# Performance work log

Measured on AMD Instinct MI355X. Metric: run time of the kernel, lower is better.

Reference implementation:

```python
import jax, jax.numpy as jnp
import numpy as np

PS = 8        # window/patch size (win_size)
STRIDE = 4    # overlapping-window stride
HEADS = 2


def _rel_pos_index(ps):
    ch = np.arange(ps)
    coords = np.stack(np.meshgrid(ch, ch, indexing='ij'))  # (2, ps, ps)
    cf = coords.reshape(2, -1)
    rel = cf[:, :, None] - cf[:, None, :]                   # (2, L, L)
    rel = rel.transpose(1, 2, 0).copy()
    rel[:, :, 0] += ps - 1
    rel[:, :, 1] += ps - 1
    rel[:, :, 0] *= 2 * ps - 1
    return rel.sum(-1).astype(np.int32)                     # (L, L)


def setup_inputs() -> dict:
    key = jax.random.key(0)
    ks = jax.random.split(key, 6)
    t, h, w, c = 8, 128, 128, 32
    inp = {
        'x': jax.random.normal(ks[0], (t, h, w, c), jnp.float32),
        'qkv_w': jax.random.normal(ks[1], (3 * c, c), jnp.float32) * (c ** -0.5),
        'qkv_b': jnp.zeros((3 * c,), jnp.float32),
        'rel_pos_table': jax.random.normal(ks[2], ((2 * PS - 1) ** 2, HEADS), jnp.float32) * 0.02,
        'proj_w': jax.random.normal(ks[3], (c, c), jnp.float32) * (c ** -0.5),
        'proj_b': jnp.zeros((c,), jnp.float32),
        'rel_pos_index': jnp.asarray(_rel_pos_index(PS)),
    }
    return inp


def reference(x, qkv_w, qkv_b, rel_pos_table, proj_w, proj_b, rel_pos_index):
    t, h, w, c = x.shape
    hd = c // HEADS
    scale = hd ** -0.5
    L = PS * PS
    nh = (h - 1) // STRIDE + 1
    nw = (w - 1) // STRIDE + 1

    # --- iUnfold: gather overlapping ps x ps patches with reflected borders ---
    r0 = jnp.arange(nh) * STRIDE
    c0 = jnp.arange(nw) * STRIDE
    ridx = r0[:, None] + jnp.arange(PS)[None, :]            # (nh, ps)
    cidx = c0[:, None] + jnp.arange(PS)[None, :]            # (nw, ps)
    ridx = jnp.where(ridx >= h, 2 * (h - 1) - ridx, ridx)
    cidx = jnp.where(cidx >= w, 2 * (w - 1) - cidx, cidx)
    # advanced indexing -> (t, nh, nw, ps, ps, c)
    patches = x[:, ridx[:, None, :, None], cidx[None, :, None, :], :]
    n = t * nh * nw
    patches = patches.reshape(n, L, c)

    # --- LinearProjection qkv ---
    qkv = patches @ qkv_w.T + qkv_b                          # (n, L, 3c)
    q, k, v = jnp.split(qkv, 3, axis=-1)
    def heads(a):
        return a.reshape(n, L, HEADS, hd).transpose(0, 2, 1, 3)  # (n, H, L, hd)
    q, k, v = heads(q), heads(k), heads(v)

    # --- scaled attention + indexed relative position bias ---
    attn = jnp.einsum('nhld,nhmd->nhlm', q * scale, k)       # (n, H, L, L)
    bias = rel_pos_table[rel_pos_index]                      # (L, L, H)
    attn = jax.nn.softmax(attn + bias.transpose(2, 0, 1)[None], axis=-1)
    out = jnp.einsum('nhlm,nhmd->nhld', attn, v)             # (n, H, L, hd)
    out = out.transpose(0, 2, 1, 3).reshape(n, L, c)
    out = out @ proj_w.T + proj_b

    # --- iFold: scatter-add with overlap-count (wfold) normalization ---
    lin = (ridx[:, None, :, None] * w + cidx[None, :, None, :]).reshape(-1)  # (nh*nw*L,)
    vals = out.reshape(t, nh * nw * L, c)
    vid = jnp.zeros((t, h * w, c), x.dtype).at[:, lin, :].add(vals)
    cnt = jnp.zeros((h * w,), x.dtype).at[lin].add(1.0)
    vid = vid / (cnt[None, :, None] + 1e-10)
    return vid.reshape(t, h, w, c)
```

## Files before the change

### kernel.cpp

```cpp
#include <hip/hip_runtime.h>
#include <hip/hip_bf16.h>
#include <stdint.h>

typedef __attribute__((ext_vector_type(8))) short bf16x8;
typedef __attribute__((ext_vector_type(4))) float f32x4;

#define LOG2E 1.44269504088896340736f
#define QSCALE (0.25f * LOG2E)

#define WS_BIASF 0u
#define WS_QKVW  32768u
#define WS_PROJW 38912u
#define WS_QKVB  40960u
#define WS_OUT   41472u
#define NEED_FULL (41472ull + 8192ull*64*32*2)

#define PWAVE 4096

__device__ __forceinline__ uint32_t pk2(float a, float b){
    union{__hip_bfloat162 h;uint32_t u;}c;
    c.h=__float22bfloat162_rn(make_float2(a,b)); return c.u;
}
template<int OFF>
__device__ __forceinline__ uint2 tr16(uint32_t a){
    uint2 d;
    asm volatile("ds_read_b64_tr_b16 %0, %1 offset:%2" : "=v"(d) : "v"(a), "i"(OFF) : "memory");
    return d;
}
__device__ __forceinline__ void lgkm0(){
    asm volatile("s_waitcnt lgkmcnt(0)" ::: "memory");
    __builtin_amdgcn_sched_barrier(0);
}
__device__ __forceinline__ bf16x8 mk8u(uint2 a, uint2 b){
    union{bf16x8 v;uint32_t u[4];}z; z.u[0]=a.x; z.u[1]=a.y; z.u[2]=b.x; z.u[3]=b.y; return z.v;
}
__device__ __forceinline__ bf16x8 mk8q(uint32_t q0, uint32_t q1, uint32_t q2, uint32_t q3){
    union{bf16x8 v;uint32_t u[4];}z; z.u[0]=q0; z.u[1]=q1; z.u[2]=q2; z.u[3]=q3; return z.v;
}
__device__ __forceinline__ void pl32(uint32_t &a, uint32_t &b){
    asm volatile("v_permlane32_swap_b32 %0, %1" : "+v"(a), "+v"(b));
}
__device__ __forceinline__ void pl16(uint32_t &a, uint32_t &b){
    asm volatile("v_permlane16_swap_b32 %0, %1" : "+v"(a), "+v"(b));
}
__device__ __forceinline__ f32x4 mfma16(uint2 a, uint2 b, f32x4 c){
    asm("v_mfma_f32_16x16x16_bf16 %0, %1, %2, %0" : "+v"(c) : "v"(a), "v"(b));
    return c;
}

__global__ __launch_bounds__(256) void prep(const float* __restrict__ qkv_w,
                                            const float* __restrict__ qkv_b,
                                            const float* __restrict__ rel_tab,
                                            const float* __restrict__ proj_w,
                                            char* __restrict__ ws)
{
    int t = blockIdx.x*256 + threadIdx.x;
    if (t < 2048) {
        int lanei = t & 63, tile = t >> 6;
        int h = tile >> 4, nt = (tile >> 2) & 3, mt = tile & 3;
        int gg = lanei >> 4, lnn = lanei & 15;
        int l = 16*nt + lnn;
        f32x4 v;
        #pragma unroll
        for (int r = 0; r < 4; ++r) {
            int m = 16*mt + 4*gg + r;
            int dr = (l >> 3) - (m >> 3) + 7;
            int dc = (l & 7) - (m & 7) + 7;
            v[r] = rel_tab[(dr*15 + dc)*2 + h] * LOG2E;
        }
        *(f32x4*)(ws + WS_BIASF + (size_t)t*16) = v;
    } else if (t < 3584) {
        int e = (t - 2048) * 2;
        int row = e >> 5;
        float s = (row < 32) ? QSCALE : 1.0f;
        *(uint32_t*)(ws + WS_QKVW + e*2) = pk2(qkv_w[e]*s, qkv_w[e+1]*s);
    } else {
        int e = (t - 3584) * 2;
        *(uint32_t*)(ws + WS_PROJW + e*2) = pk2(proj_w[e], proj_w[e+1]);
    }
    if (t < 96) {
        float s = (t < 32) ? QSCALE : 1.0f;
        ((float*)(ws + WS_QKVB))[t] = qkv_b[t] * s;
    }
}

template<int WSPATH>
__global__ __launch_bounds__(128, 3) void win_attn(
    const float* __restrict__ x, const float* __restrict__ proj_b,
    const char* __restrict__ wsc, uint16_t* __restrict__ wout,
    float* __restrict__ out)
{
    __shared__ __align__(16) char smem_all[2*PWAVE];
    const int tid = threadIdx.x;
    const int wv = tid >> 6, lane = tid & 63;
    const int g = lane >> 4, ln = lane & 15;
    const int bid = blockIdx.x;
    const int sb = (bid & 7) * 512 + (bid >> 3);
    const int wid = sb * 2 + wv;
    const int t_i = wid >> 10, wi = (wid >> 5) & 31, wj = wid & 31;
    char* smem = smem_all + wv * PWAVE;
    const uint32_t Lb = (uint32_t)(uintptr_t)(&smem[0]);

    const f32x4* biasF = (const f32x4*)(wsc + WS_BIASF);
    const uint16_t* wbf = (const uint16_t*)(wsc + WS_QKVW);
    const float* qbs = (const float*)(wsc + WS_QKVB);

    int pixb[4];
    #pragma unroll
    for (int i = 0; i < 4; ++i) {
        int tok = 16*i + ln, pr = tok >> 3, pc = tok & 7;
        int ar = wi*4 + pr; if (ar >= 128) ar = 254 - ar;
        int ac = wj*4 + pc; if (ac >= 128) ac = 254 - ac;
        pixb[i] = (t_i*128 + ar)*128 + ac;
    }

    bf16x8 xf[4];
    #pragma unroll
    for (int nt = 0; nt < 4; ++nt) {
        const float4* p = (const float4*)(x + (size_t)pixb[nt]*32 + 8*g);
        float4 a = p[0], b = p[1];
        union{bf16x8 v; uint32_t u[4];} z;
        z.u[0]=pk2(a.x,a.y); z.u[1]=pk2(a.z,a.w);
        z.u[2]=pk2(b.x,b.y); z.u[3]=pk2(b.z,b.w);
        xf[nt] = z.v;
    }

    uint2 qk[4][4];
    #pragma unroll
    for (int mt = 0; mt < 6; ++mt) {
        bf16x8 wf = *(const bf16x8*)(wbf + (ln + 16*mt)*32 + 8*g);
        float4 qb = *(const float4*)(qbs + 16*mt + 4*g);
        #pragma unroll
        for (int nt = 0; nt < 4; ++nt) {
            f32x4 acc = {qb.x, qb.y, qb.z, qb.w};
            acc = __builtin_amdgcn_mfma_f32_16x16x32_bf16(wf, xf[nt], acc, 0, 0, 0);
            if (mt < 4) {
                qk[mt][nt].x = pk2(acc[0], acc[1]);
                qk[mt][nt].y = pk2(acc[2], acc[3]);
            } else {
                int tok = 16*nt + ln;
                uint2 u; u.x = pk2(acc[0], acc[1]); u.y = pk2(acc[2], acc[3]);
                *(uint2*)(smem + (mt-4)*2048 + tok*32 + 8*g) = u;
            }
        }
    }

    const uint32_t one2 = 0x3f803f80u;
    const bf16x8 ones = mk8q(one2, one2, one2, one2);

    #pragma unroll
    for (int h = 0; h < 2; ++h) {
        f32x4 bp[16];
        #pragma unroll
        for (int t2 = 0; t2 < 16; ++t2)
            bp[t2] = biasF[(h*16 + t2)*64 + lane];

        uint32_t va = Lb + h*2048 + 256*g + 8*ln;
        uint2 v00 = tr16<0>(va),    v01 = tr16<128>(va);
        uint2 v10 = tr16<1024>(va), v11 = tr16<1152>(va);
        lgkm0();
        bf16x8 vb0 = mk8u(v00, v01), vb1 = mk8u(v10, v11);

        #pragma unroll
        for (int nt = 0; nt < 4; ++nt) {
            __builtin_amdgcn_s_setprio(1);
            f32x4 sc[4];
            #pragma unroll
            for (int mt = 0; mt < 4; ++mt)
                sc[mt] = mfma16(qk[2+h][mt], qk[h][nt], bp[nt*4 + mt]);
            __builtin_amdgcn_s_setprio(0);

            #pragma unroll
            for (int mt = 0; mt < 4; ++mt) {
                sc[mt][0]=__builtin_amdgcn_exp2f(sc[mt][0]);
                sc[mt][1]=__builtin_amdgcn_exp2f(sc[mt][1]);
                sc[mt][2]=__builtin_amdgcn_exp2f(sc[mt][2]);
                sc[mt][3]=__builtin_amdgcn_exp2f(sc[mt][3]);
            }

            uint32_t pkA[4], pkB[4];
            #pragma unroll
            for (int mt = 0; mt < 4; ++mt) {
                pkA[mt] = pk2(sc[mt][0], sc[mt][1]);
                pkB[mt] = pk2(sc[mt][2], sc[mt][3]);
            }
            uint32_t a0 = pkA[0], a1 = pkA[1]; pl32(a0, a1); pl16(a0, a1);
            uint32_t b0 = pkB[0], b1 = pkB[1]; pl32(b0, b1); pl16(b0, b1);
            bf16x8 pa0 = mk8q(a0, b0, a1, b1);
            uint32_t a2 = pkA[2], a3 = pkA[3]; pl32(a2, a3); pl16(a2, a3);
            uint32_t b2 = pkB[2], b3 = pkB[3]; pl32(b2, b3); pl16(b2, b3);
            bf16x8 pa1 = mk8q(a2, b2, a3, b3);

            __builtin_amdgcn_s_setprio(1);
            f32x4 z = {0.f,0.f,0.f,0.f};
            z = __builtin_amdgcn_mfma_f32_16x16x32_bf16(pa0, vb0, z, 0, 0, 0);
            f32x4 oc = __builtin_amdgcn_mfma_f32_16x16x32_bf16(pa1, vb1, z, 0, 0, 0);
            f32x4 sm = {0.f,0.f,0.f,0.f};
            sm = __builtin_amdgcn_mfma_f32_16x16x32_bf16(pa0, ones, sm, 0, 0, 0);
            sm = __builtin_amdgcn_mfma_f32_16x16x32_bf16(pa1, ones, sm, 0, 0, 0);
            __builtin_amdgcn_s_setprio(0);

            oc[0] *= __builtin_amdgcn_rcpf(sm[0]);
            oc[1] *= __builtin_amdgcn_rcpf(sm[1]);
            oc[2] *= __builtin_amdgcn_rcpf(sm[2]);
            oc[3] *= __builtin_amdgcn_rcpf(sm[3]);

            uint2 u; u.x = pk2(oc[0], oc[1]); u.y = pk2(oc[2], oc[3]);
            *(uint2*)(smem + h*2048 + (nt*4 + (ln>>2))*128 + (ln&3)*32 + 8*g) = u;
        }
    }

    uint32_t ob = Lb + ((uint32_t)(g >> 1) << 11) + ((uint32_t)(g & 1) << 8) + 8*ln;
    uint2 a0=tr16<0>(ob),    a1=tr16<128>(ob);
    uint2 b0=tr16<512>(ob),  b1=tr16<640>(ob);
    uint2 c0=tr16<1024>(ob), c1=tr16<1152>(ob);
    uint2 d0=tr16<1536>(ob), d1=tr16<1664>(ob);
    lgkm0();
    bf16x8 oa[4];
    oa[0]=mk8u(a0,a1); oa[1]=mk8u(b0,b1); oa[2]=mk8u(c0,c1); oa[3]=mk8u(d0,d1);

    if (WSPATH) {
        #pragma unroll
        for (int nt = 0; nt < 4; ++nt)
            *(bf16x8*)(wout + ((size_t)wid*64 + 16*nt + ln)*32 + 8*g) = oa[nt];
    } else {
        const uint16_t* pwbf = (const uint16_t*)(wsc + WS_PROJW);
        bf16x8 w2f[2];
        w2f[0] = *(const bf16x8*)(pwbf + ln*32 + 8*g);
        w2f[1] = *(const bf16x8*)(pwbf + (16 + ln)*32 + 8*g);
        float4 pbv[2];
        pbv[0] = *(const float4*)(proj_b + 4*g);
        pbv[1] = *(const float4*)(proj_b + 16 + 4*g);
        #pragma unroll
        for (int mt2 = 0; mt2 < 2; ++mt2) {
            #pragma unroll
            for (int nt = 0; nt < 4; ++nt) {
                f32x4 acc = {pbv[mt2].x, pbv[mt2].y, pbv[mt2].z, pbv[mt2].w};
                acc = __builtin_amdgcn_mfma_f32_16x16x32_bf16(w2f[mt2], oa[nt], acc, 0, 0, 0);
                #pragma unroll
                for (int r = 0; r < 4; ++r)
                    atomicAdd(out + (size_t)pixb[nt]*32 + 16*mt2 + 4*g + r, acc[r]);
            }
        }
    }
}

__global__ __launch_bounds__(256) void finish_kernel(const uint16_t* __restrict__ ws,
                                                     const char* __restrict__ wsc,
                                                     const float* __restrict__ proj_b,
                                                     float* __restrict__ out)
{
    __shared__ __align__(16) char smem[20480];
    const int tid = threadIdx.x;
    const int wv = tid >> 6, lane = tid & 63;
    const int g = lane >> 4, ln = lane & 15;
    const int pix0 = (blockIdx.x * 4 + wv) * 64;
    const int p = pix0 + lane;
    const int c = p & 127, r = (p >> 7) & 127, t_i = p >> 14;
    char* Ls = smem + wv * 5120;

    float s[32];
    #pragma unroll
    for (int q = 0; q < 32; ++q) s[q] = 0.f;

    int wr[3], pr[3], nr = 0;
    { int w0 = r >> 2;
      wr[0]=w0; pr[0]=r&3; nr=1;
      if (w0 >= 1) { wr[nr]=w0-1; pr[nr]=(r&3)+4; nr++; }
      if (r >= 123 && r <= 126) { wr[nr]=31; pr[nr]=130-r; nr++; } }
    int wc[3], pc[3], nc = 0;
    { int w0 = c >> 2;
      wc[0]=w0; pc[0]=c&3; nc=1;
      if (w0 >= 1) { wc[nc]=w0-1; pc[nc]=(c&3)+4; nc++; }
      if (c >= 123 && c <= 126) { wc[nc]=31; pc[nc]=130-c; nc++; } }

    #pragma unroll
    for (int i = 0; i < 3; ++i) {
        #pragma unroll
        for (int j = 0; j < 3; ++j) {
            if (i < nr && j < nc) {
                int win = t_i*1024 + wr[i]*32 + wc[j];
                int tok = pr[i]*8 + pc[j];
                const uint32_t* ab = (const uint32_t*)(ws + ((size_t)win*64 + tok)*32);
                #pragma unroll
                for (int q = 0; q < 16; ++q) {
                    uint32_t u = ab[q];
                    union{uint32_t uu; float f;} lo, hi;
                    lo.uu = u << 16; hi.uu = u & 0xffff0000u;
                    s[2*q]   += lo.f;
                    s[2*q+1] += hi.f;
                }
            }
        }
    }
    float inv = __builtin_amdgcn_rcpf((float)(nr*nc));
    #pragma unroll
    for (int q = 0; q < 4; ++q) {
        uint4 u;
        u.x = pk2(s[8*q+0]*inv, s[8*q+1]*inv);
        u.y = pk2(s[8*q+2]*inv, s[8*q+3]*inv);
        u.z = pk2(s[8*q+4]*inv, s[8*q+5]*inv);
        u.w = pk2(s[8*q+6]*inv, s[8*q+7]*inv);
        *(uint4*)(Ls + lane*80 + 16*q) = u;
    }
    __syncthreads();
    const uint16_t* pwbf = (const uint16_t*)(wsc + WS_PROJW);
    bf16x8 w2f[2];
    w2f[0] = *(const bf16x8*)(pwbf + ln*32 + 8*g);
    w2f[1] = *(const bf16x8*)(pwbf + (16 + ln)*32 + 8*g);
    float4 pbv[2];
    pbv[0] = *(const float4*)(proj_b + 4*g);
    pbv[1] = *(const float4*)(proj_b + 16 + 4*g);
    bf16x8 oa[4];
    #pragma unroll
    for (int nt = 0; nt < 4; ++nt)
        oa[nt] = *(const bf16x8*)(Ls + (ln + 16*nt)*80 + 16*g);
    #pragma unroll
    for (int mt2 = 0; mt2 < 2; ++mt2) {
        #pragma unroll
        for (int nt = 0; nt < 4; ++nt) {
            f32x4 acc = {pbv[mt2].x, pbv[mt2].y, pbv[mt2].z, pbv[mt2].w};
            acc = __builtin_amdgcn_mfma_f32_16x16x32_bf16(w2f[mt2], oa[nt], acc, 0, 0, 0);
            *(f32x4*)(out + (size_t)(pix0 + 16*nt + ln)*32 + 16*mt2 + 4*g) = acc;
        }
    }
}

__global__ __launch_bounds__(256) void div_kernel(float* __restrict__ out)
{
    int gid = blockIdx.x*blockDim.x + threadIdx.x;
    const int total4 = 8*128*128*32/4;
    if (gid >= total4) return;
    int pix = gid >> 3;
    int c_ = pix % 128;
    int r_ = (pix / 128) % 128;
    int cr = 0, cc = 0;
    for (int i = 0; i < 32; ++i) {
        #pragma unroll
        for (int p = 0; p < 8; ++p) {
            int rr = i*4 + p; if (rr >= 128) rr = 254 - rr;
            cr += (rr == r_);
            int aa = i*4 + p; if (aa >= 128) aa = 254 - aa;
            cc += (aa == c_);
        }
    }
    float inv = 1.f / ((float)cr*(float)cc + 1e-10f);
    float4* p4 = reinterpret_cast<float4*>(out) + gid;
    float4 v = *p4;
    v.x *= inv; v.y *= inv; v.z *= inv; v.w *= inv;
    *p4 = v;
}

extern "C" void kernel_launch(void* const* d_in, const int* in_sizes, int n_in,
                              void* d_out, int out_size, void* d_ws, size_t ws_size,
                              hipStream_t stream) {
    const float* x       = (const float*)d_in[0];
    const float* qkv_w   = (const float*)d_in[1];
    const float* qkv_b   = (const float*)d_in[2];
    const float* rel_tab = (const float*)d_in[3];
    const float* proj_w  = (const float*)d_in[4];
    const float* proj_b  = (const float*)d_in[5];
    float* out = (float*)d_out;
    char* ws = (char*)d_ws;

    prep<<<16, 256, 0, stream>>>(qkv_w, qkv_b, rel_tab, proj_w, ws);

    if (ws_size >= NEED_FULL) {
        win_attn<1><<<4096, 128, 0, stream>>>(x, proj_b, (const char*)ws,
                                              (uint16_t*)(ws + WS_OUT), out);
        finish_kernel<<<512, 256, 0, stream>>>((const uint16_t*)(ws + WS_OUT),
                                               (const char*)ws, proj_b, out);
    } else {
        hipMemsetAsync(out, 0, (size_t)out_size*sizeof(float), stream);
        win_attn<0><<<4096, 128, 0, stream>>>(x, proj_b, (const char*)ws, nullptr, out);
        const int tot4 = 8*128*128*32/4;
        div_kernel<<<(tot4 + 255)/256, 256, 0, stream>>>(out);
    }
}
```

Baseline: 51.20 us.

## Process two windows per wave and fold V bias after softmax normalization

Each wave now handles two attention windows instead of one. Weight fragments and relative-position bias loads are shared across both windows, and bias loads are software-prefetched one tile ahead instead of all 16 being held in registers. The V bias is dropped from the V projection and added after normalization, which is exact because softmax rows sum to one. Registers per wave roughly double, so launch bounds drop to 2 blocks per SIMD and the grid is halved, trading occupancy for more independent MFMA work per wave.

```diff
diff --git a/kernel.cpp b/kernel.cpp
--- a/kernel.cpp
+++ b/kernel.cpp
@@ -15,7 +15,7 @@
 #define WS_OUT   41472u
 #define NEED_FULL (41472ull + 8192ull*64*32*2)
 
-#define PWAVE 4096
+#define PWIN 4096
 
 __device__ __forceinline__ uint32_t pk2(float a, float b){
     union{__hip_bfloat162 h;uint32_t u;}c;
@@ -85,62 +85,76 @@
 }
 
 template<int WSPATH>
-__global__ __launch_bounds__(128, 3) void win_attn(
+__global__ __launch_bounds__(128, 2) void win_attn(
     const float* __restrict__ x, const float* __restrict__ proj_b,
     const char* __restrict__ wsc, uint16_t* __restrict__ wout,
     float* __restrict__ out)
 {
-    __shared__ __align__(16) char smem_all[2*PWAVE];
+    __shared__ __align__(16) char smem_all[4*PWIN];
     const int tid = threadIdx.x;
     const int wv = tid >> 6, lane = tid & 63;
     const int g = lane >> 4, ln = lane & 15;
     const int bid = blockIdx.x;
-    const int sb = (bid & 7) * 512 + (bid >> 3);
-    const int wid = sb * 2 + wv;
-    const int t_i = wid >> 10, wi = (wid >> 5) & 31, wj = wid & 31;
-    char* smem = smem_all + wv * PWAVE;
-    const uint32_t Lb = (uint32_t)(uintptr_t)(&smem[0]);
+    const int sb = (bid & 7) * 256 + (bid >> 3);
+    const int wid0 = sb*4 + wv*2;
+    char* wbase = smem_all + wv * 2 * PWIN;
+    const uint32_t Lb = (uint32_t)(uintptr_t)(&wbase[0]);
 
     const f32x4* biasF = (const f32x4*)(wsc + WS_BIASF);
     const uint16_t* wbf = (const uint16_t*)(wsc + WS_QKVW);
     const float* qbs = (const float*)(wsc + WS_QKVB);
 
-    int pixb[4];
-    #pragma unroll
-    for (int i = 0; i < 4; ++i) {
-        int tok = 16*i + ln, pr = tok >> 3, pc = tok & 7;
-        int ar = wi*4 + pr; if (ar >= 128) ar = 254 - ar;
-        int ac = wj*4 + pc; if (ac >= 128) ac = 254 - ac;
-        pixb[i] = (t_i*128 + ar)*128 + ac;
-    }
-
-    bf16x8 xf[4];
-    #pragma unroll
-    for (int nt = 0; nt < 4; ++nt) {
-        const float4* p = (const float4*)(x + (size_t)pixb[nt]*32 + 8*g);
-        float4 a = p[0], b = p[1];
-        union{bf16x8 v; uint32_t u[4];} z;
-        z.u[0]=pk2(a.x,a.y); z.u[1]=pk2(a.z,a.w);
-        z.u[2]=pk2(b.x,b.y); z.u[3]=pk2(b.z,b.w);
-        xf[nt] = z.v;
-    }
-
-    uint2 qk[4][4];
+    int pixb[2][4];
+    #pragma unroll
+    for (int w = 0; w < 2; ++w) {
+        const int wid = wid0 + w;
+        const int t_i = wid >> 10, wi = (wid >> 5) & 31, wj = wid & 31;
+        #pragma unroll
+        for (int i = 0; i < 4; ++i) {
+            int tok = 16*i + ln, pr = tok >> 3, pc = tok & 7;
+            int ar = wi*4 + pr; if (ar >= 128) ar = 254 - ar;
+            int ac = wj*4 + pc; if (ac >= 128) ac = 254 - ac;
+            pixb[w][i] = (t_i*128 + ar)*128 + ac;
+        }
+    }
+
+    bf16x8 xf[2][4];
+    #pragma unroll
+    for (int w = 0; w < 2; ++w) {
+        #pragma unroll
+        for (int nt = 0; nt < 4; ++nt) {
+            const float4* p = (const float4*)(x + (size_t)pixb[w][nt]*32 + 8*g);
+            float4 a = p[0], b = p[1];
+            union{bf16x8 v; uint32_t u[4];} z;
+            z.u[0]=pk2(a.x,a.y); z.u[1]=pk2(a.z,a.w);
+            z.u[2]=pk2(b.x,b.y); z.u[3]=pk2(b.z,b.w);
+            xf[w][nt] = z.v;
+        }
+    }
+
+    const f32x4 zero4 = {0.f, 0.f, 0.f, 0.f};
+
+    uint2 qk[2][4][4];
     #pragma unroll
     for (int mt = 0; mt < 6; ++mt) {
         bf16x8 wf = *(const bf16x8*)(wbf + (ln + 16*mt)*32 + 8*g);
         float4 qb = *(const float4*)(qbs + 16*mt + 4*g);
         #pragma unroll
-        for (int nt = 0; nt < 4; ++nt) {
-            f32x4 acc = {qb.x, qb.y, qb.z, qb.w};
-            acc = __builtin_amdgcn_mfma_f32_16x16x32_bf16(wf, xf[nt], acc, 0, 0, 0);
-            if (mt < 4) {
-                qk[mt][nt].x = pk2(acc[0], acc[1]);
-                qk[mt][nt].y = pk2(acc[2], acc[3]);
-            } else {
-                int tok = 16*nt + ln;
-                uint2 u; u.x = pk2(acc[0], acc[1]); u.y = pk2(acc[2], acc[3]);
-                *(uint2*)(smem + (mt-4)*2048 + tok*32 + 8*g) = u;
+        for (int w = 0; w < 2; ++w) {
+            #pragma unroll
+            for (int nt = 0; nt < 4; ++nt) {
+                f32x4 acc;
+                if (mt < 4) { acc[0]=qb.x; acc[1]=qb.y; acc[2]=qb.z; acc[3]=qb.w; }
+                else        { acc = zero4; }
+                acc = __builtin_amdgcn_mfma_f32_16x16x32_bf16(wf, xf[w][nt], acc, 0, 0, 0);
+                if (mt < 4) {
+                    qk[w][mt][nt].x = pk2(acc[0], acc[1]);
+                    qk[w][mt][nt].y = pk2(acc[2], acc[3]);
+                } else {
+                    int tok = 16*nt + ln;
+                    uint2 u; u.x = pk2(acc[0], acc[1]); u.y = pk2(acc[2], acc[3]);
+                    *(uint2*)(wbase + w*PWIN + (mt-4)*2048 + tok*32 + 8*g) = u;
+                }
             }
         }
     }
@@ -150,96 +164,130 @@
 
     #pragma unroll
     for (int h = 0; h < 2; ++h) {
-        f32x4 bp[16];
-        #pragma unroll
-        for (int t2 = 0; t2 < 16; ++t2)
-            bp[t2] = biasF[(h*16 + t2)*64 + lane];
-
-        uint32_t va = Lb + h*2048 + 256*g + 8*ln;
-        uint2 v00 = tr16<0>(va),    v01 = tr16<128>(va);
-        uint2 v10 = tr16<1024>(va), v11 = tr16<1152>(va);
+        const float bvh = qbs[64 + 16*h + ln];
+
+        uint2 vr[2][4];
+        #pragma unroll
+        for (int w = 0; w < 2; ++w) {
+            uint32_t va = Lb + w*PWIN + h*2048 + 256*g + 8*ln;
+            vr[w][0] = tr16<0>(va);    vr[w][1] = tr16<128>(va);
+            vr[w][2] = tr16<1024>(va); vr[w][3] = tr16<1152>(va);
+        }
         lgkm0();
-        bf16x8 vb0 = mk8u(v00, v01), vb1 = mk8u(v10, v11);
+        bf16x8 vb0[2], vb1[2];
+        #pragma unroll
+        for (int w = 0; w < 2; ++w) {
+            vb0[w] = mk8u(vr[w][0], vr[w][1]);
+            vb1[w] = mk8u(vr[w][2], vr[w][3]);
+        }
+
+        f32x4 bpc[4];
+        #pragma unroll
+        for (int mt = 0; mt < 4; ++mt)
+            bpc[mt] = biasF[(h*16 + 0*4 + mt)*64 + lane];
 
         #pragma unroll
         for (int nt = 0; nt < 4; ++nt) {
+            f32x4 bpn[4];
+            const int ntn = (nt < 3) ? nt + 1 : 3;
+            #pragma unroll
+            for (int mt = 0; mt < 4; ++mt)
+                bpn[mt] = biasF[(h*16 + ntn*4 + mt)*64 + lane];
+
             __builtin_amdgcn_s_setprio(1);
-            f32x4 sc[4];
-            #pragma unroll
-            for (int mt = 0; mt < 4; ++mt)
-                sc[mt] = mfma16(qk[2+h][mt], qk[h][nt], bp[nt*4 + mt]);
+            f32x4 sc[2][4];
+            #pragma unroll
+            for (int w = 0; w < 2; ++w)
+                #pragma unroll
+                for (int mt = 0; mt < 4; ++mt)
+                    sc[w][mt] = mfma16(qk[w][2+h][mt], qk[w][h][nt], bpc[mt]);
             __builtin_amdgcn_s_setprio(0);
 
             #pragma unroll
-            for (int mt = 0; mt < 4; ++mt) {
-                sc[mt][0]=__builtin_amdgcn_exp2f(sc[mt][0]);
-                sc[mt][1]=__builtin_amdgcn_exp2f(sc[mt][1]);
-                sc[mt][2]=__builtin_amdgcn_exp2f(sc[mt][2]);
-                sc[mt][3]=__builtin_amdgcn_exp2f(sc[mt][3]);
+            for (int w = 0; w < 2; ++w)
+                #pragma unroll
+                for (int mt = 0; mt < 4; ++mt) {
+                    sc[w][mt][0]=__builtin_amdgcn_exp2f(sc[w][mt][0]);
+                    sc[w][mt][1]=__builtin_amdgcn_exp2f(sc[w][mt][1]);
+                    sc[w][mt][2]=__builtin_amdgcn_exp2f(sc[w][mt][2]);
+                    sc[w][mt][3]=__builtin_amdgcn_exp2f(sc[w][mt][3]);
+                }
+
+            #pragma unroll
+            for (int w = 0; w < 2; ++w) {
+                uint32_t pkA[4], pkB[4];
+                #pragma unroll
+                for (int mt = 0; mt < 4; ++mt) {
+                    pkA[mt] = pk2(sc[w][mt][0], sc[w][mt][1]);
+                    pkB[mt] = pk2(sc[w][mt][2], sc[w][mt][3]);
+                }
+                uint32_t a0 = pkA[0], a1 = pkA[1]; pl32(a0, a1); pl16(a0, a1);
+                uint32_t b0 = pkB[0], b1 = pkB[1]; pl32(b0, b1); pl16(b0, b1);
+                bf16x8 pa0 = mk8q(a0, b0, a1, b1);
+                uint32_t a2 = pkA[2], a3 = pkA[3]; pl32(a2, a3); pl16(a2, a3);
+                uint32_t b2 = pkB[2], b3 = pkB[3]; pl32(b2, b3); pl16(b2, b3);
+                bf16x8 pa1 = mk8q(a2, b2, a3, b3);
+
+                __builtin_amdgcn_s_setprio(1);
+                f32x4 z = __builtin_amdgcn_mfma_f32_16x16x32_bf16(pa0, vb0[w], zero4, 0, 0, 0);
+                f32x4 oc = __builtin_amdgcn_mfma_f32_16x16x32_bf16(pa1, vb1[w], z, 0, 0, 0);
+                f32x4 sm = __builtin_amdgcn_mfma_f32_16x16x32_bf16(pa0, ones, zero4, 0, 0, 0);
+                sm = __builtin_amdgcn_mfma_f32_16x16x32_bf16(pa1, ones, sm, 0, 0, 0);
+                __builtin_amdgcn_s_setprio(0);
+
+                oc[0] = oc[0]*__builtin_amdgcn_rcpf(sm[0]) + bvh;
+                oc[1] = oc[1]*__builtin_amdgcn_rcpf(sm[1]) + bvh;
+                oc[2] = oc[2]*__builtin_amdgcn_rcpf(sm[2]) + bvh;
+                oc[3] = oc[3]*__builtin_amdgcn_rcpf(sm[3]) + bvh;
+
+                uint2 u; u.x = pk2(oc[0], oc[1]); u.y = pk2(oc[2], oc[3]);
+                *(uint2*)(wbase + w*PWIN + h*2048 + (nt*4 + (ln>>2))*128 + (ln&3)*32 + 8*g) = u;
             }
 
-            uint32_t pkA[4], pkB[4];
-            #pragma unroll
-            for (int mt = 0; mt < 4; ++mt) {
-                pkA[mt] = pk2(sc[mt][0], sc[mt][1]);
-                pkB[mt] = pk2(sc[mt][2], sc[mt][3]);
-            }
-            uint32_t a0 = pkA[0], a1 = pkA[1]; pl32(a0, a1); pl16(a0, a1);
-            uint32_t b0 = pkB[0], b1 = pkB[1]; pl32(b0, b1); pl16(b0, b1);
-            bf16x8 pa0 = mk8q(a0, b0, a1, b1);
-            uint32_t a2 = pkA[2], a3 = pkA[3]; pl32(a2, a3); pl16(a2, a3);
-            uint32_t b2 = pkB[2], b3 = pkB[3]; pl32(b2, b3); pl16(b2, b3);
-            bf16x8 pa1 = mk8q(a2, b2, a3, b3);
-
-            __builtin_amdgcn_s_setprio(1);
-            f32x4 z = {0.f,0.f,0.f,0.f};
-            z = __builtin_amdgcn_mfma_f32_16x16x32_bf16(pa0, vb0, z, 0, 0, 0);
-            f32x4 oc = __builtin_amdgcn_mfma_f32_16x16x32_bf16(pa1, vb1, z, 0, 0, 0);
-            f32x4 sm = {0.f,0.f,0.f,0.f};
-            sm = __builtin_amdgcn_mfma_f32_16x16x32_bf16(pa0, ones, sm, 0, 0, 0);
-            sm = __builtin_amdgcn_mfma_f32_16x16x32_bf16(pa1, ones, sm, 0, 0, 0);
-            __builtin_amdgcn_s_setprio(0);
-
-            oc[0] *= __builtin_amdgcn_rcpf(sm[0]);
-            oc[1] *= __builtin_amdgcn_rcpf(sm[1]);
-            oc[2] *= __builtin_amdgcn_rcpf(sm[2]);
-            oc[3] *= __builtin_amdgcn_rcpf(sm[3]);
-
-            uint2 u; u.x = pk2(oc[0], oc[1]); u.y = pk2(oc[2], oc[3]);
-            *(uint2*)(smem + h*2048 + (nt*4 + (ln>>2))*128 + (ln&3)*32 + 8*g) = u;
-        }
-    }
-
-    uint32_t ob = Lb + ((uint32_t)(g >> 1) << 11) + ((uint32_t)(g & 1) << 8) + 8*ln;
-    uint2 a0=tr16<0>(ob),    a1=tr16<128>(ob);
-    uint2 b0=tr16<512>(ob),  b1=tr16<640>(ob);
-    uint2 c0=tr16<1024>(ob), c1=tr16<1152>(ob);
-    uint2 d0=tr16<1536>(ob), d1=tr16<1664>(ob);
+            #pragma unroll
+            for (int mt = 0; mt < 4; ++mt) bpc[mt] = bpn[mt];
+        }
+    }
+
+    uint2 orr[2][8];
+    #pragma unroll
+    for (int w = 0; w < 2; ++w) {
+        uint32_t ob = Lb + w*PWIN + ((uint32_t)(g >> 1) << 11) + ((uint32_t)(g & 1) << 8) + 8*ln;
+        orr[w][0]=tr16<0>(ob);    orr[w][1]=tr16<128>(ob);
+        orr[w][2]=tr16<512>(ob);  orr[w][3]=tr16<640>(ob);
+        orr[w][4]=tr16<1024>(ob); orr[w][5]=tr16<1152>(ob);
+        orr[w][6]=tr16<1536>(ob); orr[w][7]=tr16<1664>(ob);
+    }
     lgkm0();
-    bf16x8 oa[4];
-    oa[0]=mk8u(a0,a1); oa[1]=mk8u(b0,b1); oa[2]=mk8u(c0,c1); oa[3]=mk8u(d0,d1);
-
-    if (WSPATH) {
-        #pragma unroll
-        for (int nt = 0; nt < 4; ++nt)
-            *(bf16x8*)(wout + ((size_t)wid*64 + 16*nt + ln)*32 + 8*g) = oa[nt];
-    } else {
-        const uint16_t* pwbf = (const uint16_t*)(wsc + WS_PROJW);
-        bf16x8 w2f[2];
-        w2f[0] = *(const bf16x8*)(pwbf + ln*32 + 8*g);
-        w2f[1] = *(const bf16x8*)(pwbf + (16 + ln)*32 + 8*g);
-        float4 pbv[2];
-        pbv[0] = *(const float4*)(proj_b + 4*g);
-        pbv[1] = *(const float4*)(proj_b + 16 + 4*g);
-        #pragma unroll
-        for (int mt2 = 0; mt2 < 2; ++mt2) {
-            #pragma unroll
-            for (int nt = 0; nt < 4; ++nt) {
-                f32x4 acc = {pbv[mt2].x, pbv[mt2].y, pbv[mt2].z, pbv[mt2].w};
-                acc = __builtin_amdgcn_mfma_f32_16x16x32_bf16(w2f[mt2], oa[nt], acc, 0, 0, 0);
+
+    #pragma unroll
+    for (int w = 0; w < 2; ++w) {
+        const int wid = wid0 + w;
+        bf16x8 oa[4];
+        oa[0]=mk8u(orr[w][0],orr[w][1]); oa[1]=mk8u(orr[w][2],orr[w][3]);
+        oa[2]=mk8u(orr[w][4],orr[w][5]); oa[3]=mk8u(orr[w][6],orr[w][7]);
+        if (WSPATH) {
+            #pragma unroll
+            for (int nt = 0; nt < 4; ++nt)
+                *(bf16x8*)(wout + ((size_t)wid*64 + 16*nt + ln)*32 + 8*g) = oa[nt];
+        } else {
+            const uint16_t* pwbf = (const uint16_t*)(wsc + WS_PROJW);
+            bf16x8 w2f[2];
+            w2f[0] = *(const bf16x8*)(pwbf + ln*32 + 8*g);
+            w2f[1] = *(const bf16x8*)(pwbf + (16 + ln)*32 + 8*g);
+            float4 pbv[2];
+            pbv[0] = *(const float4*)(proj_b + 4*g);
+            pbv[1] = *(const float4*)(proj_b + 16 + 4*g);
+            #pragma unroll
+            for (int mt2 = 0; mt2 < 2; ++mt2) {
                 #pragma unroll
-                for (int r = 0; r < 4; ++r)
-                    atomicAdd(out + (size_t)pixb[nt]*32 + 16*mt2 + 4*g + r, acc[r]);
+                for (int nt = 0; nt < 4; ++nt) {
+                    f32x4 acc = {pbv[mt2].x, pbv[mt2].y, pbv[mt2].z, pbv[mt2].w};
+                    acc = __builtin_amdgcn_mfma_f32_16x16x32_bf16(w2f[mt2], oa[nt], acc, 0, 0, 0);
+                    #pragma unroll
+                    for (int r = 0; r < 4; ++r)
+                        atomicAdd(out + (size_t)pixb[w][nt]*32 + 16*mt2 + 4*g + r, acc[r]);
+                }
             }
         }
     }
@@ -366,13 +414,13 @@
     prep<<<16, 256, 0, stream>>>(qkv_w, qkv_b, rel_tab, proj_w, ws);
 
     if (ws_size >= NEED_FULL) {
-        win_attn<1><<<4096, 128, 0, stream>>>(x, proj_b, (const char*)ws,
+        win_attn<1><<<2048, 128, 0, stream>>>(x, proj_b, (const char*)ws,
                                               (uint16_t*)(ws + WS_OUT), out);
         finish_kernel<<<512, 256, 0, stream>>>((const uint16_t*)(ws + WS_OUT),
                                                (const char*)ws, proj_b, out);
     } else {
         hipMemsetAsync(out, 0, (size_t)out_size*sizeof(float), stream);
-        win_attn<0><<<4096, 128, 0, stream>>>(x, proj_b, (const char*)ws, nullptr, out);
+        win_attn<0><<<2048, 128, 0, stream>>>(x, proj_b, (const char*)ws, nullptr, out);
         const int tot4 = 8*128*128*32/4;
         div_kernel<<<(tot4 + 255)/256, 256, 0, stream>>>(out);
     }
```

Measured after the change: 54.89 us. 1.07x slower.
